# Kernel tuning notes

Hardware: AMD Instinct MI355X
Metric: run time of the kernel (lower is better)

## Reference

```python
import jax, jax.numpy as jnp
import numpy as np

N_WIRES = 4
BATCH, SEQ, EMBED, FFN = 8, 512, 512, 2048


def setup_inputs() -> dict:
    key = jax.random.key(0)
    k_x, k_w1, k_w2 = jax.random.split(key, 3)
    x = jax.random.normal(k_x, (BATCH, SEQ, EMBED), dtype=jnp.float32)
    # Linear params (torch Linear: y = x @ W^T + b; we store pre-transposed)
    W1 = jax.random.normal(k_w1, (EMBED, FFN), dtype=jnp.float32) / np.sqrt(EMBED)
    b1 = jnp.zeros((FFN,), dtype=jnp.float32)
    W2 = jax.random.normal(k_w2, (FFN, EMBED), dtype=jnp.float32) / np.sqrt(FFN)
    b2 = jnp.zeros((EMBED,), dtype=jnp.float32)
    return {"x": x, "W1": W1, "b1": b1, "W2": W2, "b2": b2}


def reference(x, W1, b1, W2, b2):
    b, s, d = x.shape
    flat = x.reshape(b * s, d)                      # [n, d], n = b*s
    # Quantum kernel: circuit RY(x_i) then RY(-y_i) per wire on |0..0>;
    # |0..0> amplitude = prod_i cos((x_i - y_i)/2); only first n_wires feats used
    # (reset_states(1) + states.view(-1)[0] selects batch row 0 of the reshape).
    f = flat[:, :N_WIRES]                           # [n, nw]
    half_diff = (f[:, None, :] - f[None, :, :]) * 0.5   # [n, n, nw]
    gram = jnp.abs(jnp.prod(jnp.cos(half_diff), axis=-1))  # [n, n]
    out = gram @ flat                               # [n, d]
    h = jax.nn.relu(out @ W1 + b1)                  # [n, ffn]  (dropout = eval identity)
    y = h @ W2 + b2                                 # [n, d]
    return y.reshape(b, s, d)
```

## Files before the change

### kernel.cpp

```cpp
#include <hip/hip_runtime.h>
#include <hip/hip_bf16.h>
#include <stdint.h>

using bf = __bf16;
typedef __attribute__((ext_vector_type(8))) __bf16 bf16x8;
typedef __attribute__((ext_vector_type(4))) float f32x4;
typedef __attribute__((ext_vector_type(4))) int i32x4;

#define M_TOT 4096
#define D_EMB 512
#define F_FFN 2048

__device__ __forceinline__ void gload_lds16(const void* g, void* l) {
  __builtin_amdgcn_global_load_lds(
      (const __attribute__((address_space(1))) uint32_t*)g,
      (__attribute__((address_space(3))) uint32_t*)l, 16, 0, 0);
}

__device__ __forceinline__ int swz128(int row, int b) {
  return row * 128 + (b ^ ((row & 7) << 4));
}
__device__ __forceinline__ bf16x8 ldf128(const char* base, int row, int b) {
  return *(const bf16x8*)(base + swz128(row, b));
}
__device__ __forceinline__ i32x4 ldf128i(const char* base, int row, int b) {
  return *(const i32x4*)(base + swz128(row, b));
}
template <int CHUNKS>
__device__ __forceinline__ void stage_rows8(const void* gsrc, size_t ld_bytes, char* lbase,
                                            int wave, int lane) {
  const int rsub = lane >> 3, csub = lane & 7;
  const int sc = csub ^ rsub;
#pragma unroll
  for (int i = 0; i < CHUNKS / 8; ++i) {
    int chunk = wave + i * 8;
    int row = chunk * 8 + rsub;
    gload_lds16((const char*)gsrc + (size_t)row * ld_bytes + sc * 16, lbase + chunk * 1024);
  }
}

__device__ __forceinline__ int quant_i8(float x, float s) {
  float v = x * s;
  v = fminf(127.f, fmaxf(-127.f, v));
  return (int)rintf(v);
}

__device__ __forceinline__ void do_transpose_bf(const float* __restrict__ in, bf* __restrict__ out,
                                                int R, int C, int tileIdx, int tid, float tile[32][33]) {
  int tilesX = C / 32;
  int c0 = (tileIdx % tilesX) * 32, r0 = (tileIdx / tilesX) * 32;
  int tx = tid & 31, ty = tid >> 5;
#pragma unroll
  for (int i = 0; i < 32; i += 8)
    tile[ty + i][tx] = in[(size_t)(r0 + ty + i) * C + c0 + tx];
  __syncthreads();
#pragma unroll
  for (int i = 0; i < 32; i += 8)
    out[(size_t)(c0 + ty + i) * R + r0 + tx] = (bf)tile[tx][ty + i];
}

#define NT_FT  2048
#define NT_W1  1024
#define NT_W2  1024
#define NT_PHI 16

__global__ __launch_bounds__(256) void k_prep(const float* __restrict__ x,
                                              const float* __restrict__ W1,
                                              const float* __restrict__ W2,
                                              int8_t* __restrict__ fi8, bf* __restrict__ w1T,
                                              bf* __restrict__ w2T, bf* __restrict__ phib) {
  __shared__ float tile[32][33];
  const int bid = blockIdx.x, tid = threadIdx.x;
  if (bid < NT_FT) {
    int c0 = (bid % (D_EMB / 32)) * 32, r0 = (bid / (D_EMB / 32)) * 32;
    int tx = tid & 31, ty = tid >> 5;
#pragma unroll
    for (int i = 0; i < 32; i += 8)
      tile[ty + i][tx] = x[(size_t)(r0 + ty + i) * D_EMB + c0 + tx];
    __syncthreads();
#pragma unroll
    for (int i = 0; i < 32; i += 8)
      fi8[(size_t)(c0 + ty + i) * M_TOT + r0 + tx] = (int8_t)quant_i8(tile[tx][ty + i], 15.875f);
  } else if (bid < NT_FT + NT_W1) {
    do_transpose_bf(W1, w1T, D_EMB, F_FFN, bid - NT_FT, tid, tile);
  } else if (bid < NT_FT + NT_W1 + NT_W2) {
    do_transpose_bf(W2, w2T, F_FFN, D_EMB, bid - NT_FT - NT_W1, tid, tile);
  } else {
    int i = (bid - NT_FT - NT_W1 - NT_W2) * 256 + tid;
    float c[4], s[4];
#pragma unroll
    for (int k = 0; k < 4; ++k) {
      float f = x[(size_t)i * D_EMB + k] * 0.5f;
      sincosf(f, &s[k], &c[k]);
    }
#pragma unroll
    for (int m = 0; m < 16; ++m) {
      float p = 1.0f;
#pragma unroll
      for (int k = 0; k < 4; ++k) p *= ((m >> k) & 1) ? s[k] : c[k];
      phib[(size_t)i * 32 + m] = (bf)p;
    }
#pragma unroll
    for (int m = 16; m < 32; ++m) phib[(size_t)i * 32 + m] = (bf)0.0f;
  }
}

__global__ __launch_bounds__(256, 4) void k_sgen(const bf* __restrict__ phib, int8_t* __restrict__ S) {
  __shared__ __align__(16) char st[16384];
  const int lin = blockIdx.x;
  const int m0 = (lin & 31) * 128;
  const int j0 = (lin >> 5) * 128;
  const int tid = threadIdx.x;
  const int wave = tid >> 6, lane = tid & 63;
  const int lr = lane & 15, lg = lane >> 4;

  const bf* pm = phib + (size_t)(m0 + wave * 32) * 32;
  const bf16x8 a0 = *(const bf16x8*)(pm + (size_t)lr * 32 + lg * 8);
  const bf16x8 a1 = *(const bf16x8*)(pm + (size_t)(16 + lr) * 32 + lg * 8);

  const int mb0 = wave * 32 + lg * 4;
  const int key = (lr & 7) << 4;
#pragma unroll
  for (int jf = 0; jf < 8; ++jf) {
    bf16x8 b = *(const bf16x8*)(phib + (size_t)(j0 + jf * 16 + lr) * 32 + lg * 8);
    f32x4 s0 = __builtin_amdgcn_mfma_f32_16x16x32_bf16(a0, b, f32x4{0.f, 0.f, 0.f, 0.f}, 0, 0, 0);
    f32x4 s1 = __builtin_amdgcn_mfma_f32_16x16x32_bf16(a1, b, f32x4{0.f, 0.f, 0.f, 0.f}, 0, 0, 0);
    uint32_t w0 = 0, w1 = 0;
#pragma unroll
    for (int r = 0; r < 4; ++r) {
      uint32_t q0 = (uint32_t)min(127, (int)rintf(fabsf(s0[r]) * 127.f));
      uint32_t q1 = (uint32_t)min(127, (int)rintf(fabsf(s1[r]) * 127.f));
      w0 |= q0 << (8 * r);
      w1 |= q1 << (8 * r);
    }
    int jrow = jf * 16 + lr;
    *(uint32_t*)(st + jrow * 128 + (mb0 ^ key)) = w0;
    *(uint32_t*)(st + jrow * 128 + ((mb0 + 16) ^ key)) = w1;
  }
  __syncthreads();
#pragma unroll
  for (int i = 0; i < 4; ++i) {
    int idx = tid + i * 256;
    int jrow = idx >> 3, seg = idx & 7;
    i32x4 v = *(const i32x4*)(st + jrow * 128 + ((seg * 16) ^ ((jrow & 7) << 4)));
    *(i32x4*)(S + (size_t)(j0 + jrow) * M_TOT + m0 + seg * 16) = v;
  }
}

__global__ __launch_bounds__(512, 1) void k_gemmi8(const int8_t* __restrict__ S,
                                                   const int8_t* __restrict__ FT,
                                                   bf* __restrict__ outb) {
  constexpr int ABUF = 64 * 128, BBUF = 128 * 128, BUF = ABUF + BBUF;
  __shared__ __align__(16) char sm[3 * BUF];

  const int tid = threadIdx.x;
  const int wave = tid >> 6, lane = tid & 63;
  const int lr = lane & 15, lg = lane >> 4;
  const int wm = wave & 1, wn = (wave >> 1) & 1, ks = wave >> 2;

  const int lin = blockIdx.x;
  const int e = lin & 7, jj = lin >> 3;
  const int bm = e * 8 + (jj >> 2), bn = jj & 3;
  const int m0 = bm * 64, n0 = bn * 128;

  i32x4 acc[2][4];
#pragma unroll
  for (int i = 0; i < 2; ++i)
#pragma unroll
    for (int f = 0; f < 4; ++f) acc[i][f] = i32x4{0, 0, 0, 0};

  stage_rows8<8>(S + (size_t)m0 * M_TOT, M_TOT, sm, wave, lane);
  stage_rows8<16>(FT + (size_t)n0 * M_TOT, M_TOT, sm + ABUF, wave, lane);
  stage_rows8<8>(S + (size_t)m0 * M_TOT + 128, M_TOT, sm + BUF, wave, lane);
  stage_rows8<16>(FT + (size_t)n0 * M_TOT + 128, M_TOT, sm + BUF + ABUF, wave, lane);

  constexpr int NT = M_TOT / 128;
  for (int t = 0; t < NT; ++t) {
    char* aTc = sm + (t % 3) * BUF;
    char* bTc = aTc + ABUF;
    if (t + 1 < NT) asm volatile("s_waitcnt vmcnt(3)" ::: "memory");
    else            asm volatile("s_waitcnt vmcnt(0)" ::: "memory");
    __builtin_amdgcn_s_barrier();

    if (t + 2 < NT) {
      char* aTn = sm + ((t + 2) % 3) * BUF;
      stage_rows8<8>(S + (size_t)m0 * M_TOT + (t + 2) * 128, M_TOT, aTn, wave, lane);
      stage_rows8<16>(FT + (size_t)n0 * M_TOT + (t + 2) * 128, M_TOT, aTn + ABUF, wave, lane);
    }
    i32x4 a[2], b[4];
#pragma unroll
    for (int i = 0; i < 2; ++i) a[i] = ldf128i(aTc, wm * 32 + i * 16 + lr, ks * 64 + lg * 16);
#pragma unroll
    for (int f = 0; f < 4; ++f) b[f] = ldf128i(bTc, wn * 64 + f * 16 + lr, ks * 64 + lg * 16);
#pragma unroll
    for (int i = 0; i < 2; ++i)
#pragma unroll
      for (int f = 0; f < 4; ++f)
        acc[i][f] = __builtin_amdgcn_mfma_i32_16x16x64_i8(a[i], b[f], acc[i][f], 0, 0, 0);
  }

  __syncthreads();
  if (ks == 1) {
    char* dst = sm + (wave - 4) * 8192 + lane * 128;
#pragma unroll
    for (int i = 0; i < 2; ++i)
#pragma unroll
      for (int f = 0; f < 4; ++f) *(i32x4*)(dst + (i * 4 + f) * 16) = acc[i][f];
  }
  __syncthreads();
  if (ks == 0) {
    const char* src = sm + wave * 8192 + lane * 128;
    constexpr float SCALE = 8.0f / 16129.0f;
#pragma unroll
    for (int i = 0; i < 2; ++i)
#pragma unroll
      for (int f = 0; f < 4; ++f) {
        i32x4 p = *(const i32x4*)(src + (i * 4 + f) * 16);
        int n = n0 + wn * 64 + f * 16 + lr;
#pragma unroll
        for (int r = 0; r < 4; ++r) {
          int m = m0 + wm * 32 + i * 16 + lg * 4 + r;
          outb[(size_t)m * D_EMB + n] = (bf)((float)(acc[i][f][r] + p[r]) * SCALE);
        }
      }
  }
}

template <int BM, int BN, int OUTMODE>
__global__ __launch_bounds__(512, 1) void k_gemm8(const bf* __restrict__ A, const bf* __restrict__ BT,
                                                  const float* __restrict__ bias, void* __restrict__ out,
                                                  int M, int N, int K) {
  constexpr int WN = BN / 2;
  constexpr int FM = 2, FN = WN / 16;
  constexpr int ABUF = BM * 128, BBUF = BN * 128, BUF = ABUF + BBUF;
  constexpr int LP = BM / 64 + BN / 64;
  static_assert(LP == 3 || LP == 4, "vmcnt literal");
  __shared__ __align__(16) char sm[3 * BUF];

  const int tid = threadIdx.x;
  const int wave = tid >> 6, lane = tid & 63;
  const int lr = lane & 15, lg = lane >> 4;
  const int wm = wave >> 1, wn = wave & 1;

  const int lin = blockIdx.x;
  const int e = lin & 7, jj = lin >> 3;
  const int nbn = N / BN;
  const int bm = e * 4 + jj / nbn, bn = jj % nbn;
  const int m0 = bm * BM, n0 = bn * BN;

  f32x4 acc[FM][FN];
#pragma unroll
  for (int i = 0; i < FM; ++i)
#pragma unroll
    for (int f = 0; f < FN; ++f) acc[i][f] = f32x4{0.f, 0.f, 0.f, 0.f};

  stage_rows8<BM / 8>(A + (size_t)m0 * K, (size_t)K * 2, sm, wave, lane);
  stage_rows8<BN / 8>(BT + (size_t)n0 * K, (size_t)K * 2, sm + ABUF, wave, lane);
  stage_rows8<BM / 8>(A + (size_t)m0 * K + 64, (size_t)K * 2, sm + BUF, wave, lane);
  stage_rows8<BN / 8>(BT + (size_t)n0 * K + 64, (size_t)K * 2, sm + BUF + ABUF, wave, lane);

  const int NT = K / 64;
  for (int t = 0; t < NT; ++t) {
    char* aTc = sm + (t % 3) * BUF;
    char* bTc = aTc + ABUF;
    if (t + 1 < NT) {
      if constexpr (LP == 3) asm volatile("s_waitcnt vmcnt(3)" ::: "memory");
      else                   asm volatile("s_waitcnt vmcnt(4)" ::: "memory");
    } else {
      asm volatile("s_waitcnt vmcnt(0)" ::: "memory");
    }
    __builtin_amdgcn_s_barrier();

    if (t + 2 < NT) {
      char* aTn = sm + ((t + 2) % 3) * BUF;
      stage_rows8<BM / 8>(A + (size_t)m0 * K + (t + 2) * 64, (size_t)K * 2, aTn, wave, lane);
      stage_rows8<BN / 8>(BT + (size_t)n0 * K + (t + 2) * 64, (size_t)K * 2, aTn + ABUF, wave, lane);
    }
#pragma unroll
    for (int ksl = 0; ksl < 2; ++ksl) {
      bf16x8 a[FM], b[FN];
#pragma unroll
      for (int i = 0; i < FM; ++i) a[i] = ldf128(aTc, wm * 32 + i * 16 + lr, (ksl * 32 + lg * 8) * 2);
#pragma unroll
      for (int f = 0; f < FN; ++f) b[f] = ldf128(bTc, wn * WN + f * 16 + lr, (ksl * 32 + lg * 8) * 2);
#pragma unroll
      for (int i = 0; i < FM; ++i)
#pragma unroll
        for (int f = 0; f < FN; ++f)
          acc[i][f] = __builtin_amdgcn_mfma_f32_16x16x32_bf16(a[i], b[f], acc[i][f], 0, 0, 0);
    }
  }

#pragma unroll
  for (int f = 0; f < FN; ++f) {
    int n = n0 + wn * WN + f * 16 + lr;
    float bv = (OUTMODE == 2) ? 0.f : bias[n];
#pragma unroll
    for (int i = 0; i < FM; ++i)
#pragma unroll
      for (int r = 0; r < 4; ++r) {
        int m = m0 + wm * 32 + i * 16 + lg * 4 + r;
        float v = acc[i][f][r] + bv;
        if (OUTMODE == 1) {
          v = v > 0.f ? v : 0.f;
          ((bf*)out)[(size_t)m * N + n] = (bf)v;
        } else {
          ((float*)out)[(size_t)m * N + n] = v;
        }
      }
  }
}

constexpr size_t OFF_PHI  = 0;
constexpr size_t OFF_FI8  = OFF_PHI + (size_t)M_TOT * 32 * 2;
constexpr size_t OFF_OUTB = OFF_FI8 + (size_t)D_EMB * M_TOT;
constexpr size_t OFF_W1T  = OFF_OUTB + (size_t)M_TOT * D_EMB * 2;
constexpr size_t OFF_W2T  = OFF_W1T + (size_t)F_FFN * D_EMB * 2;
constexpr size_t OFF_S    = OFF_W2T + (size_t)D_EMB * F_FFN * 2;
constexpr size_t OFF_HB   = OFF_S;

extern "C" void kernel_launch(void* const* d_in, const int* in_sizes, int n_in,
                              void* d_out, int out_size, void* d_ws, size_t ws_size,
                              hipStream_t stream) {
  const float* x  = (const float*)d_in[0];
  const float* W1 = (const float*)d_in[1];
  const float* b1 = (const float*)d_in[2];
  const float* W2 = (const float*)d_in[3];
  const float* b2 = (const float*)d_in[4];
  float* y = (float*)d_out;
  char* ws = (char*)d_ws;

  bf* phib    = (bf*)(ws + OFF_PHI);
  int8_t* fi8 = (int8_t*)(ws + OFF_FI8);
  bf* outb    = (bf*)(ws + OFF_OUTB);
  bf* w1T     = (bf*)(ws + OFF_W1T);
  bf* w2T     = (bf*)(ws + OFF_W2T);
  int8_t* S   = (int8_t*)(ws + OFF_S);
  bf* hb      = (bf*)(ws + OFF_HB);

  k_prep<<<dim3(NT_FT + NT_W1 + NT_W2 + NT_PHI), 256, 0, stream>>>(x, W1, W2, fi8, w1T, w2T, phib);

  k_sgen<<<dim3(1024), 256, 0, stream>>>(phib, S);
  k_gemmi8<<<dim3(256), 512, 0, stream>>>(S, fi8, outb);

  k_gemm8<128, 128, 1><<<dim3(512), 512, 0, stream>>>(outb, w1T, b1, (void*)hb, M_TOT, F_FFN, D_EMB);
  k_gemm8<128, 64, 0><<<dim3(256), 512, 0, stream>>>(hb, w2T, b2, (void*)y, M_TOT, D_EMB, F_FFN);
}
```

Baseline: 68.15 us.

## Fuse phi/S generation into prep kernel and retile FFN1 GEMM to 256-thread blocks

The separate S-generation kernel and phi buffer are removed. Each of 1024 new prep blocks now computes phi for its 128+128 rows into LDS and emits its S tile, alongside the transpose blocks, which saves one launch and the phi round trip through global memory. The first FFN GEMM switches from the 512-thread 128x128 k_gemm8 to a new 256-thread 128x64 kernel with 1024 blocks and two blocks per CU, aiming for better occupancy and wave balance. The cost is some redundant sincos work per block (each row's phi is recomputed by many blocks) and a larger LDS footprint in prep, which may limit occupancy of the transpose blocks.

```diff
diff --git a/kernel.cpp b/kernel.cpp
--- a/kernel.cpp
+++ b/kernel.cpp
@@ -38,6 +38,18 @@
     gload_lds16((const char*)gsrc + (size_t)row * ld_bytes + sc * 16, lbase + chunk * 1024);
   }
 }
+template <int CHUNKS>
+__device__ __forceinline__ void stage_rows4(const void* gsrc, size_t ld_bytes, char* lbase,
+                                            int wave, int lane) {
+  const int rsub = lane >> 3, csub = lane & 7;
+  const int sc = csub ^ rsub;
+#pragma unroll
+  for (int i = 0; i < CHUNKS / 4; ++i) {
+    int chunk = wave + i * 4;
+    int row = chunk * 8 + rsub;
+    gload_lds16((const char*)gsrc + (size_t)row * ld_bytes + sc * 16, lbase + chunk * 1024);
+  }
+}
 
 __device__ __forceinline__ int quant_i8(float x, float s) {
   float v = x * s;
@@ -45,35 +57,85 @@
   return (int)rintf(v);
 }
 
-__device__ __forceinline__ void do_transpose_bf(const float* __restrict__ in, bf* __restrict__ out,
-                                                int R, int C, int tileIdx, int tid, float tile[32][33]) {
-  int tilesX = C / 32;
-  int c0 = (tileIdx % tilesX) * 32, r0 = (tileIdx / tilesX) * 32;
-  int tx = tid & 31, ty = tid >> 5;
-#pragma unroll
-  for (int i = 0; i < 32; i += 8)
-    tile[ty + i][tx] = in[(size_t)(r0 + ty + i) * C + c0 + tx];
-  __syncthreads();
-#pragma unroll
-  for (int i = 0; i < 32; i += 8)
-    out[(size_t)(c0 + ty + i) * R + r0 + tx] = (bf)tile[tx][ty + i];
-}
-
-#define NT_FT  2048
-#define NT_W1  1024
-#define NT_W2  1024
-#define NT_PHI 16
+#define NB_SGEN 1024
+#define NT_FT   2048
+#define NT_W1   1024
+#define NT_W2   1024
 
 __global__ __launch_bounds__(256) void k_prep(const float* __restrict__ x,
                                               const float* __restrict__ W1,
                                               const float* __restrict__ W2,
                                               int8_t* __restrict__ fi8, bf* __restrict__ w1T,
-                                              bf* __restrict__ w2T, bf* __restrict__ phib) {
-  __shared__ float tile[32][33];
+                                              bf* __restrict__ w2T, int8_t* __restrict__ S) {
+  __shared__ __align__(16) char smem[32768];
   const int bid = blockIdx.x, tid = threadIdx.x;
-  if (bid < NT_FT) {
-    int c0 = (bid % (D_EMB / 32)) * 32, r0 = (bid / (D_EMB / 32)) * 32;
-    int tx = tid & 31, ty = tid >> 5;
+
+  if (bid < NB_SGEN) {
+    char* phiL = smem;
+    char* st = smem + 16384;
+    const int m0 = (bid & 31) * 128;
+    const int j0 = (bid >> 5) * 128;
+    {
+      int g = (tid < 128) ? (m0 + tid) : (j0 + tid - 128);
+      float c[4], s[4];
+#pragma unroll
+      for (int k = 0; k < 4; ++k) {
+        float f = x[(size_t)g * D_EMB + k] * 0.5f;
+        sincosf(f, &s[k], &c[k]);
+      }
+      bf* row = (bf*)(phiL + tid * 64);
+#pragma unroll
+      for (int m = 0; m < 16; ++m) {
+        float p = 1.0f;
+#pragma unroll
+        for (int k = 0; k < 4; ++k) p *= ((m >> k) & 1) ? s[k] : c[k];
+        row[m] = (bf)p;
+      }
+#pragma unroll
+      for (int m = 16; m < 32; ++m) row[m] = (bf)0.0f;
+    }
+    __syncthreads();
+
+    const int wave = tid >> 6, lane = tid & 63;
+    const int lr = lane & 15, lg = lane >> 4;
+    const bf16x8 a0 = *(const bf16x8*)(phiL + (wave * 32 + lr) * 64 + lg * 16);
+    const bf16x8 a1 = *(const bf16x8*)(phiL + (wave * 32 + 16 + lr) * 64 + lg * 16);
+
+    const int mb0 = wave * 32 + lg * 4;
+    const int key = (lr & 7) << 4;
+#pragma unroll
+    for (int jf = 0; jf < 8; ++jf) {
+      bf16x8 b = *(const bf16x8*)(phiL + (128 + jf * 16 + lr) * 64 + lg * 16);
+      f32x4 s0 = __builtin_amdgcn_mfma_f32_16x16x32_bf16(a0, b, f32x4{0.f, 0.f, 0.f, 0.f}, 0, 0, 0);
+      f32x4 s1 = __builtin_amdgcn_mfma_f32_16x16x32_bf16(a1, b, f32x4{0.f, 0.f, 0.f, 0.f}, 0, 0, 0);
+      uint32_t w0 = 0, w1 = 0;
+#pragma unroll
+      for (int r = 0; r < 4; ++r) {
+        uint32_t q0 = (uint32_t)min(127, (int)rintf(fabsf(s0[r]) * 127.f));
+        uint32_t q1 = (uint32_t)min(127, (int)rintf(fabsf(s1[r]) * 127.f));
+        w0 |= q0 << (8 * r);
+        w1 |= q1 << (8 * r);
+      }
+      int jrow = jf * 16 + lr;
+      *(uint32_t*)(st + jrow * 128 + (mb0 ^ key)) = w0;
+      *(uint32_t*)(st + jrow * 128 + ((mb0 + 16) ^ key)) = w1;
+    }
+    __syncthreads();
+#pragma unroll
+    for (int i = 0; i < 4; ++i) {
+      int idx = tid + i * 256;
+      int jrow = idx >> 3, seg = idx & 7;
+      i32x4 v = *(const i32x4*)(st + jrow * 128 + ((seg * 16) ^ ((jrow & 7) << 4)));
+      *(i32x4*)(S + (size_t)(j0 + jrow) * M_TOT + m0 + seg * 16) = v;
+    }
+    return;
+  }
+
+  float(*tile)[33] = (float(*)[33])smem;
+  const int tx = tid & 31, ty = tid >> 5;
+  if (bid < NB_SGEN + NT_FT) {
+    int b2 = bid - NB_SGEN;
+    int c0 = (b2 % (D_EMB / 32)) * 32, r0 = (b2 / (D_EMB / 32)) * 32;
 #pragma unroll
     for (int i = 0; i < 32; i += 8)
       tile[ty + i][tx] = x[(size_t)(r0 + ty + i) * D_EMB + c0 + tx];
@@ -81,69 +143,26 @@
 #pragma unroll
     for (int i = 0; i < 32; i += 8)
       fi8[(size_t)(c0 + ty + i) * M_TOT + r0 + tx] = (int8_t)quant_i8(tile[tx][ty + i], 15.875f);
-  } else if (bid < NT_FT + NT_W1) {
-    do_transpose_bf(W1, w1T, D_EMB, F_FFN, bid - NT_FT, tid, tile);
-  } else if (bid < NT_FT + NT_W1 + NT_W2) {
-    do_transpose_bf(W2, w2T, F_FFN, D_EMB, bid - NT_FT - NT_W1, tid, tile);
+  } else if (bid < NB_SGEN + NT_FT + NT_W1) {
+    int b2 = bid - NB_SGEN - NT_FT;
+    int c0 = (b2 % (F_FFN / 32)) * 32, r0 = (b2 / (F_FFN / 32)) * 32;
+#pragma unroll
+    for (int i = 0; i < 32; i += 8)
+      tile[ty + i][tx] = W1[(size_t)(r0 + ty + i) * F_FFN + c0 + tx];
+    __syncthreads();
+#pragma unroll
+    for (int i = 0; i < 32; i += 8)
+      w1T[(size_t)(c0 + ty + i) * D_EMB + r0 + tx] = (bf)tile[tx][ty + i];
   } else {
-    int i = (bid - NT_FT - NT_W1 - NT_W2) * 256 + tid;
-    float c[4], s[4];
-#pragma unroll
-    for (int k = 0; k < 4; ++k) {
-      float f = x[(size_t)i * D_EMB + k] * 0.5f;
-      sincosf(f, &s[k], &c[k]);
-    }
-#pragma unroll
-    for (int m = 0; m < 16; ++m) {
-      float p = 1.0f;
-#pragma unroll
-      for (int k = 0; k < 4; ++k) p *= ((m >> k) & 1) ? s[k] : c[k];
-      phib[(size_t)i * 32 + m] = (bf)p;
-    }
-#pragma unroll
-    for (int m = 16; m < 32; ++m) phib[(size_t)i * 32 + m] = (bf)0.0f;
-  }
-}
-
-__global__ __launch_bounds__(256, 4) void k_sgen(const bf* __restrict__ phib, int8_t* __restrict__ S) {
-  __shared__ __align__(16) char st[16384];
-  const int lin = blockIdx.x;
-  const int m0 = (lin & 31) * 128;
-  const int j0 = (lin >> 5) * 128;
-  const int tid = threadIdx.x;
-  const int wave = tid >> 6, lane = tid & 63;
-  const int lr = lane & 15, lg = lane >> 4;
-
-  const bf* pm = phib + (size_t)(m0 + wave * 32) * 32;
-  const bf16x8 a0 = *(const bf16x8*)(pm + (size_t)lr * 32 + lg * 8);
-  const bf16x8 a1 = *(const bf16x8*)(pm + (size_t)(16 + lr) * 32 + lg * 8);
-
-  const int mb0 = wave * 32 + lg * 4;
-  const int key = (lr & 7) << 4;
-#pragma unroll
-  for (int jf = 0; jf < 8; ++jf) {
-    bf16x8 b = *(const bf16x8*)(phib + (size_t)(j0 + jf * 16 + lr) * 32 + lg * 8);
-    f32x4 s0 = __builtin_amdgcn_mfma_f32_16x16x32_bf16(a0, b, f32x4{0.f, 0.f, 0.f, 0.f}, 0, 0, 0);
-    f32x4 s1 = __builtin_amdgcn_mfma_f32_16x16x32_bf16(a1, b, f32x4{0.f, 0.f, 0.f, 0.f}, 0, 0, 0);
-    uint32_t w0 = 0, w1 = 0;
-#pragma unroll
-    for (int r = 0; r < 4; ++r) {
-      uint32_t q0 = (uint32_t)min(127, (int)rintf(fabsf(s0[r]) * 127.f));
-      uint32_t q1 = (uint32_t)min(127, (int)rintf(fabsf(s1[r]) * 127.f));
-      w0 |= q0 << (8 * r);
-      w1 |= q1 << (8 * r);
-    }
-    int jrow = jf * 16 + lr;
-    *(uint32_t*)(st + jrow * 128 + (mb0 ^ key)) = w0;
-    *(uint32_t*)(st + jrow * 128 + ((mb0 + 16) ^ key)) = w1;
-  }
-  __syncthreads();
-#pragma unroll
-  for (int i = 0; i < 4; ++i) {
-    int idx = tid + i * 256;
-    int jrow = idx >> 3, seg = idx & 7;
-    i32x4 v = *(const i32x4*)(st + jrow * 128 + ((seg * 16) ^ ((jrow & 7) << 4)));
-    *(i32x4*)(S + (size_t)(j0 + jrow) * M_TOT + m0 + seg * 16) = v;
+    int b2 = bid - NB_SGEN - NT_FT - NT_W1;
+    int c0 = (b2 % (D_EMB / 32)) * 32, r0 = (b2 / (D_EMB / 32)) * 32;
+#pragma unroll
+    for (int i = 0; i < 32; i += 8)
+      tile[ty + i][tx] = W2[(size_t)(r0 + ty + i) * D_EMB + c0 + tx];
+    __syncthreads();
+#pragma unroll
+    for (int i = 0; i < 32; i += 8)
+      w2T[(size_t)(c0 + ty + i) * F_FFN + r0 + tx] = (bf)tile[tx][ty + i];
   }
 }
 
@@ -222,6 +241,78 @@
           int m = m0 + wm * 32 + i * 16 + lg * 4 + r;
           outb[(size_t)m * D_EMB + n] = (bf)((float)(acc[i][f][r] + p[r]) * SCALE);
         }
+      }
+  }
+}
+
+__global__ __launch_bounds__(256, 2) void k_gemm4(const bf* __restrict__ A, const bf* __restrict__ BT,
+                                                  const float* __restrict__ bias, bf* __restrict__ out,
+                                                  int M, int N, int K) {
+  constexpr int BM = 128, BN = 64;
+  constexpr int ABUF = BM * 128, BBUF = BN * 128, BUF = ABUF + BBUF;
+  __shared__ __align__(16) char sm[3 * BUF];
+
+  const int tid = threadIdx.x;
+  const int wave = tid >> 6, lane = tid & 63;
+  const int lr = lane & 15, lg = lane >> 4;
+  const int wm = wave >> 1, wn = wave & 1;
+
+  const int lin = blockIdx.x;
+  const int e = lin & 7, jj = lin >> 3;
+  const int bm = e * 4 + (jj & 3), bn = jj >> 2;
+  const int m0 = bm * BM, n0 = bn * BN;
+
+  f32x4 acc[4][2];
+#pragma unroll
+  for (int i = 0; i < 4; ++i)
+#pragma unroll
+    for (int f = 0; f < 2; ++f) acc[i][f] = f32x4{0.f, 0.f, 0.f, 0.f};
+
+  stage_rows4<16>(A + (size_t)m0 * K, (size_t)K * 2, sm, wave, lane);
+  stage_rows4<8>(BT + (size_t)n0 * K, (size_t)K * 2, sm + ABUF, wave, lane);
+  stage_rows4<16>(A + (size_t)m0 * K + 64, (size_t)K * 2, sm + BUF, wave, lane);
+  stage_rows4<8>(BT + (size_t)n0 * K + 64, (size_t)K * 2, sm + BUF + ABUF, wave, lane);
+
+  const int NT = K / 64;
+  for (int t = 0; t < NT; ++t) {
+    char* aTc = sm + (t % 3) * BUF;
+    char* bTc = aTc + ABUF;
+    if (t + 1 < NT) asm volatile("s_waitcnt vmcnt(6)" ::: "memory");
+    else            asm volatile("s_waitcnt vmcnt(0)" ::: "memory");
+    __builtin_amdgcn_s_barrier();
+
+    if (t + 2 < NT) {
+      char* aTn = sm + ((t + 2) % 3) * BUF;
+      stage_rows4<16>(A + (size_t)m0 * K + (t + 2) * 64, (size_t)K * 2, aTn, wave, lane);
+      stage_rows4<8>(BT + (size_t)n0 * K + (t + 2) * 64, (size_t)K * 2, aTn + ABUF, wave, lane);
+    }
+#pragma unroll
+    for (int ksl = 0; ksl < 2; ++ksl) {
+      bf16x8 a[4], b[2];
+#pragma unroll
+      for (int i = 0; i < 4; ++i) a[i] = ldf128(aTc, wm * 64 + i * 16 + lr, (ksl * 32 + lg * 8) * 2);
+#pragma unroll
+      for (int f = 0; f < 2; ++f) b[f] = ldf128(bTc, wn * 32 + f * 16 + lr, (ksl * 32 + lg * 8) * 2);
+#pragma unroll
+      for (int i = 0; i < 4; ++i)
+#pragma unroll
+        for (int f = 0; f < 2; ++f)
+          acc[i][f] = __builtin_amdgcn_mfma_f32_16x16x32_bf16(a[i], b[f], acc[i][f], 0, 0, 0);
+    }
+  }
+
+#pragma unroll
+  for (int f = 0; f < 2; ++f) {
+    int n = n0 + wn * 32 + f * 16 + lr;
+    float bv = bias[n];
+#pragma unroll
+    for (int i = 0; i < 4; ++i)
+#pragma unroll
+      for (int r = 0; r < 4; ++r) {
+        int m = m0 + wm * 64 + i * 16 + lg * 4 + r;
+        float v = acc[i][f][r] + bv;
+        v = v > 0.f ? v : 0.f;
+        out[(size_t)m * N + n] = (bf)v;
       }
   }
 }
@@ -311,8 +402,7 @@
   }
 }
 
-constexpr size_t OFF_PHI  = 0;
-constexpr size_t OFF_FI8  = OFF_PHI + (size_t)M_TOT * 32 * 2;
+constexpr size_t OFF_FI8  = 0;
 constexpr size_t OFF_OUTB = OFF_FI8 + (size_t)D_EMB * M_TOT;
 constexpr size_t OFF_W1T  = OFF_OUTB + (size_t)M_TOT * D_EMB * 2;
 constexpr size_t OFF_W2T  = OFF_W1T + (size_t)F_FFN * D_EMB * 2;
@@ -330,7 +420,6 @@
   float* y = (float*)d_out;
   char* ws = (char*)d_ws;
 
-  bf* phib    = (bf*)(ws + OFF_PHI);
   int8_t* fi8 = (int8_t*)(ws + OFF_FI8);
   bf* outb    = (bf*)(ws + OFF_OUTB);
   bf* w1T     = (bf*)(ws + OFF_W1T);
@@ -338,11 +427,10 @@
   int8_t* S   = (int8_t*)(ws + OFF_S);
   bf* hb      = (bf*)(ws + OFF_HB);
 
-  k_prep<<<dim3(NT_FT + NT_W1 + NT_W2 + NT_PHI), 256, 0, stream>>>(x, W1, W2, fi8, w1T, w2T, phib);
-
-  k_sgen<<<dim3(1024), 256, 0, stream>>>(phib, S);
+  k_prep<<<dim3(NB_SGEN + NT_FT + NT_W1 + NT_W2), 256, 0, stream>>>(x, W1, W2, fi8, w1T, w2T, S);
+
   k_gemmi8<<<dim3(256), 512, 0, stream>>>(S, fi8, outb);
 
-  k_gemm8<128, 128, 1><<<dim3(512), 512, 0, stream>>>(outb, w1T, b1, (void*)hb, M_TOT, F_FFN, D_EMB);
+  k_gemm4<<<dim3(1024), 256, 0, stream>>>(outb, w1T, b1, hb, M_TOT, F_FFN, D_EMB);
   k_gemm8<128, 64, 0><<<dim3(256), 512, 0, stream>>>(hb, w2T, b2, (void*)y, M_TOT, D_EMB, F_FFN);
 }
```

New measurement: 68.12 us. No clear change (-0.0%).
